# Performance work log

Hardware: AMD Instinct MI355X
Metric: run time of the kernel (lower is better)

The kernel has to match this reference:

```python
import jax, jax.numpy as jnp
import numpy as np

B, S, D, H = 2, 2048, 1024, 16  # batch, seq, d_model, num_heads
DH = D // H


def setup_inputs() -> dict:
    key = jax.random.key(0)
    ks = jax.random.split(key, 11)
    sc = 1.0 / np.sqrt(D)
    return {
        "q": jax.random.normal(ks[0], (B, S, D), jnp.float32),
        "k": jax.random.normal(ks[1], (B, S, D), jnp.float32),
        "v": jax.random.normal(ks[2], (B, S, D), jnp.float32),
        "wq": jax.random.normal(ks[3], (D, D), jnp.float32) * sc,
        "bq": jax.random.normal(ks[4], (D,), jnp.float32) * 0.01,
        "wk": jax.random.normal(ks[5], (D, D), jnp.float32) * sc,
        "bk": jax.random.normal(ks[6], (D,), jnp.float32) * 0.01,
        "wv": jax.random.normal(ks[7], (D, D), jnp.float32) * sc,
        "bv": jax.random.normal(ks[8], (D,), jnp.float32) * 0.01,
        "wo": jax.random.normal(ks[9], (D, D), jnp.float32) * sc,
        "bo": jax.random.normal(ks[10], (D,), jnp.float32) * 0.01,
    }


def reference(q, k, v, wq, bq, wk, bk, wv, bv, wo, bo):
    # projections: [B,S,D]
    query = q @ wq + bq
    key_ = k @ wk + bk
    value = v @ wv + bv
    # split heads: [B,H,S,DH]
    def split(x):
        return jnp.transpose(x.reshape(B, S, H, DH), (0, 2, 1, 3))
    query, key_, value = split(query), split(key_), split(value)
    # NOTE: original module applies NO 1/sqrt(d_k) scaling
    scores = jnp.einsum("bhqd,bhkd->bhqk", query, key_)
    attn = jax.nn.softmax(scores, axis=-1)
    data = jnp.einsum("bhqk,bhkd->bhqd", attn, value)  # [B,H,S,DH]
    # faithful to original bug: transpose(0,1) then view(B,S,-1)
    data = jnp.swapaxes(data, 0, 1).reshape(B, S, D)
    return data @ wo + bo
```

## Files before the change

kernel.cpp:

```cpp
#include <hip/hip_runtime.h>

typedef _Float16 f16;
typedef _Float16 f16x8 __attribute__((ext_vector_type(8)));
typedef _Float16 f16x4 __attribute__((ext_vector_type(4)));
typedef float    f32x4 __attribute__((ext_vector_type(4)));

static constexpr int BATCH = 2, SEQ = 2048, DMODEL = 1024, HEADS = 16, DHEAD = 64;
static constexpr int MTOK = BATCH * SEQ;
static constexpr float LOG2E = 1.44269504088896f;

#define GLOBAL_LOAD_LDS16(gptr, lptr)                                              \
  __builtin_amdgcn_global_load_lds(                                                \
      (const __attribute__((address_space(1))) void*)(gptr),                       \
      (__attribute__((address_space(3))) void*)(lptr), 16, 0, 0)

#define MFMA16(a, b, c) __builtin_amdgcn_mfma_f32_16x16x32_f16((a), (b), (c), 0, 0, 0)

#define WAITV_(N) asm volatile("s_waitcnt vmcnt(" #N ")" ::: "memory")
#define WAITV(N) WAITV_(N)

__device__ __forceinline__ float fexp2(float x) {
  float r;
  asm volatile("v_exp_f32 %0, %1" : "=v"(r) : "v"(x));
  return r;
}

__device__ __forceinline__ int imgAB(int mr, int kr) {
  int pr = mr >> 1;
  int jj = ((mr & 1) << 2) | (kr >> 3);
  int j = jj ^ (pr & 7);
  return pr * 64 + j * 8 + (kr & 7);
}
__device__ __forceinline__ int imgK(int sr, int dh) {
  return sr * 64 + (((dh >> 3) ^ (sr & 7)) << 3) + (dh & 7);
}

__global__ __launch_bounds__(256) void cast_kernel(const float* __restrict__ src,
                                                   f16* __restrict__ dst) {
  int c = blockIdx.x * 256 + threadIdx.x;
  int blk = c >> 8, cb = c & 255;
  int pr = cb >> 3, j = cb & 7;
  int jj = j ^ (pr & 7);
  int mr = (pr << 1) | (jj >> 2);
  int kr = (jj & 3) << 3;
  int m = (blk >> 5) * 64 + mr;
  int k = (blk & 31) * 32 + kr;
  const float* s = src + (size_t)m * DMODEL + k;
  f32x4 a = *(const f32x4*)s, b = *(const f32x4*)(s + 4);
  f16x8 o;
  o[0] = (f16)a[0]; o[1] = (f16)a[1]; o[2] = (f16)a[2]; o[3] = (f16)a[3];
  o[4] = (f16)b[0]; o[5] = (f16)b[1]; o[6] = (f16)b[2]; o[7] = (f16)b[3];
  *(f16x8*)(dst + (size_t)c * 8) = o;
}

__global__ __launch_bounds__(256) void transw_kernel(
    const float* __restrict__ w0, const float* __restrict__ w1,
    const float* __restrict__ w2, const float* __restrict__ w3,
    f16* __restrict__ Wimg) {
  const int z = blockIdx.z;
  const float* w = z == 0 ? w0 : z == 1 ? w1 : z == 2 ? w2 : w3;
  f16* t = Wimg + (size_t)z * DMODEL * DMODEL;
  __shared__ f16 lt[64][72];
  const int k0 = blockIdx.x * 64, n0 = blockIdx.y * 64;
  const int r = threadIdx.x >> 2, c0 = (threadIdx.x & 3) * 16;
  const float* src = w + (size_t)(k0 + r) * DMODEL + n0 + c0;
#pragma unroll
  for (int jx = 0; jx < 16; jx += 4) {
    f32x4 x = *(const f32x4*)(src + jx);
    lt[c0 + jx + 0][r] = (f16)x[0];
    lt[c0 + jx + 1][r] = (f16)x[1];
    lt[c0 + jx + 2][r] = (f16)x[2];
    lt[c0 + jx + 3][r] = (f16)x[3];
  }
  __syncthreads();
  const int n = n0 + r;
#pragma unroll
  for (int cw = 0; cw < 2; cw++) {
    int k = k0 + c0 + cw * 8;
    int blk = ((n >> 6) << 5) | (k >> 5);
    int off = blk * 2048 + imgAB(n & 63, k & 31);
    f16x8 v;
#pragma unroll
    for (int e = 0; e < 8; e++) v[e] = lt[r][c0 + cw * 8 + e];
    *(f16x8*)(t + off) = v;
  }
}

__global__ __launch_bounds__(256) void proj_kernel(
    const f16* __restrict__ Ximg, const f16* __restrict__ Wimg,
    const float* __restrict__ bq, const float* __restrict__ bk,
    const float* __restrict__ bv, f16* __restrict__ Qp, f16* __restrict__ Kp,
    f16* __restrict__ Vt, int zbase, size_t aStride) {
  __shared__ f16 As[2][4096];
  __shared__ f16 Bs[2][4096];
  const int z = zbase + blockIdx.z;
  const f16* A = Ximg + (size_t)blockIdx.z * aStride;
  const f16* Bw = Wimg + (size_t)z * DMODEL * DMODEL;
  int lin = blockIdx.x + (blockIdx.y << 3);
  int swz = ((lin & 7) << 5) + (lin >> 3);
  const int n0 = (swz & 7) * 128, m0 = (swz >> 3) * 128;
  const int tid = threadIdx.x, w = tid >> 6, l = tid & 63, q = l & 15, g = l >> 4;
  const int wr = w >> 1, wc = w & 1;
  const int KT = DMODEL >> 5;
  int aoff[4], boff[4];
#pragma unroll
  for (int mi = 0; mi < 4; mi++) {
    int mr = wr * 64 + mi * 16 + q;
    aoff[mi] = ((mr >> 6) << 11) + imgAB(mr & 63, g * 8);
  }
#pragma unroll
  for (int ni = 0; ni < 4; ni++) {
    int nr = wc * 64 + ni * 16 + q;
    boff[ni] = ((nr >> 6) << 11) + imgAB(nr & 63, g * 8);
  }
  f32x4 acc[4][4] = {};

#define PROJ_STAGE(bb, t)                                                          \
  {                                                                                \
    _Pragma("unroll")                                                              \
    for (int i = 0; i < 2; i++) {                                                  \
      int c = w * 2 + i;                                                           \
      size_t ga = (size_t)(((m0 >> 6) + (c >> 2)) * KT + (t)) * 2048 +             \
                  (c & 3) * 512 + l * 8;                                           \
      GLOBAL_LOAD_LDS16(A + ga, (char*)&As[bb][c * 512]);                          \
      size_t gb = (size_t)(((n0 >> 6) + (c >> 2)) * KT + (t)) * 2048 +             \
                  (c & 3) * 512 + l * 8;                                           \
      GLOBAL_LOAD_LDS16(Bw + gb, (char*)&Bs[bb][c * 512]);                         \
    }                                                                              \
  }

  PROJ_STAGE(0, 0);
  for (int t = 0; t < KT; t++) {
    const int bb = t & 1;
    if (t < KT - 1) {
      PROJ_STAGE(bb ^ 1, t + 1);
      WAITV(4);
    } else {
      WAITV(0);
    }
    __builtin_amdgcn_s_barrier();
    f16x8 af[4], bf[4];
#pragma unroll
    for (int mi = 0; mi < 4; mi++) af[mi] = *(const f16x8*)&As[bb][aoff[mi]];
#pragma unroll
    for (int ni = 0; ni < 4; ni++) bf[ni] = *(const f16x8*)&Bs[bb][boff[ni]];
#pragma unroll
    for (int mi = 0; mi < 4; mi++)
#pragma unroll
      for (int ni = 0; ni < 4; ni++)
        acc[mi][ni] = MFMA16(af[mi], bf[ni], acc[mi][ni]);
    __builtin_amdgcn_s_barrier();
  }
  const float* bias = z == 0 ? bq : (z == 1 ? bk : bv);
#pragma unroll
  for (int mi = 0; mi < 4; mi++)
#pragma unroll
    for (int ni = 0; ni < 4; ni++) {
      const int col = n0 + wc * 64 + ni * 16 + q;
      const float bvl = bias[col];
      const int row0 = m0 + wr * 64 + mi * 16 + g * 4;
      if (z == 0) {
#pragma unroll
        for (int r = 0; r < 4; r++)
          Qp[(size_t)(row0 + r) * DMODEL + col] = (f16)((acc[mi][ni][r] + bvl) * LOG2E);
      } else if (z == 1) {
        const int h = col >> 6, dh = col & 63;
#pragma unroll
        for (int r = 0; r < 4; r++) {
          const int row = row0 + r, s = row & (SEQ - 1);
          Kp[(size_t)(((row >> 11) * HEADS + h) * 64 + (s >> 5)) * 2048 + imgK(s & 31, dh)] =
              (f16)(acc[mi][ni][r] + bvl);
        }
      } else {
        const int h = col >> 6, dh = col & 63;
        const int s0 = row0 & (SEQ - 1);
        f16* dst = Vt + (size_t)(((row0 >> 11) * HEADS + h) * 64 + (s0 >> 5)) * 2048 +
                   imgAB(dh, s0 & 31);
        f16x4 ov;
        ov[0] = (f16)(acc[mi][ni][0] + bvl); ov[1] = (f16)(acc[mi][ni][1] + bvl);
        ov[2] = (f16)(acc[mi][ni][2] + bvl); ov[3] = (f16)(acc[mi][ni][3] + bvl);
        *(f16x4*)dst = ov;
      }
    }
}

__global__ __launch_bounds__(256, 4) void attn_kernel(
    const f16* __restrict__ Qp, const f16* __restrict__ Kimg,
    const f16* __restrict__ Vimg, f16* __restrict__ Simg) {
  __shared__ f16 Klds[2][2][2048];
  __shared__ f16 Vlds[2][2][2048];
  __shared__ f16 Plds[4][2][512];
  const int tid = threadIdx.x, w = tid >> 6, l = tid & 63, q = l & 15, g = l >> 4;
  const int lin = blockIdx.x;
  const int swz = ((lin & 7) << 7) + (lin >> 3);
  const int qb = swz & 31, bh = swz >> 5;
  const int b = bh >> 4, h = bh & 15;
  const int q0 = qb * 64 + w * 16;

  const f16* qrow = Qp + (size_t)(b * SEQ + q0 + q) * DMODEL + h * 64;
  const f16x8 qf0 = *(const f16x8*)(qrow + g * 8);
  const f16x8 qf1 = *(const f16x8*)(qrow + 32 + g * 8);
  const f16* kt_base = Kimg + (size_t)(bh * 64) * 2048;
  const f16* vt_base = Vimg + (size_t)(bh * 64) * 2048;

  int koff[4][2];
#pragma unroll
  for (int fn = 0; fn < 4; fn++)
#pragma unroll
    for (int hf = 0; hf < 2; hf++)
      koff[fn][hf] = (fn >> 1) * 2048 + imgK((fn & 1) * 16 + q, hf * 32 + g * 8);
  int voff[4];
#pragma unroll
  for (int fo = 0; fo < 4; fo++) voff[fo] = imgAB(fo * 16 + q, g * 8);
  const int poff = imgAB(q, g * 8);
  int pwoff[2];
  {
    const int pr = q >> 1;
#pragma unroll
    for (int fn = 0; fn < 2; fn++) {
      int jj = ((q & 1) << 2) | (fn * 2 + (g >> 1));
      pwoff[fn] = pr * 64 + ((jj ^ (pr & 7)) << 3) + (g & 1) * 4;
    }
  }
  float m_st = -1.0e30f, l_pt = 0.f;
  f32x4 o_acc[4] = {};

#define ATTN_STAGE(bb, t)                                                          \
  {                                                                                \
    const f16* sb_ = (w < 2) ? (kt_base + (size_t)(2 * (t) + w) * 2048)            \
                             : (vt_base + (size_t)(2 * (t) + (w - 2)) * 2048);     \
    f16* db_ = (w < 2) ? &Klds[bb][w][0] : &Vlds[bb][w - 2][0];                    \
    _Pragma("unroll")                                                              \
    for (int j_ = 0; j_ < 4; j_++)                                                 \
      GLOBAL_LOAD_LDS16(sb_ + j_ * 512 + l * 8, (char*)(db_ + j_ * 512));          \
  }

  ATTN_STAGE(0, 0);
  for (int t = 0; t < 32; t++) {
    const int bb = t & 1;
    if (t < 31) {
      ATTN_STAGE(bb ^ 1, t + 1);
      WAITV(4);
    } else {
      WAITV(0);
    }
    __builtin_amdgcn_s_barrier();
    const f16* Kb = &Klds[bb][0][0];
    f32x4 sacc[4];
#pragma unroll
    for (int fn = 0; fn < 4; fn++) {
      f32x4 zz = {};
      zz = MFMA16(*(const f16x8*)(Kb + koff[fn][0]), qf0, zz);
      zz = MFMA16(*(const f16x8*)(Kb + koff[fn][1]), qf1, zz);
      sacc[fn] = zz;
    }
    float lm = fmaxf(
        fmaxf(fmaxf(fmaxf(sacc[0][0], sacc[0][1]), fmaxf(sacc[0][2], sacc[0][3])),
              fmaxf(fmaxf(sacc[1][0], sacc[1][1]), fmaxf(sacc[1][2], sacc[1][3]))),
        fmaxf(fmaxf(fmaxf(sacc[2][0], sacc[2][1]), fmaxf(sacc[2][2], sacc[2][3])),
              fmaxf(fmaxf(sacc[3][0], sacc[3][1]), fmaxf(sacc[3][2], sacc[3][3]))));
    if (!__all(lm <= m_st + 8.f)) {
      float mx = fmaxf(lm, __shfl_xor(lm, 16, 64));
      mx = fmaxf(mx, __shfl_xor(mx, 32, 64));
      const float mnew = fmaxf(m_st, mx);
      const float sc = fexp2(m_st - mnew);
      m_st = mnew;
      l_pt *= sc;
#pragma unroll
      for (int fo = 0; fo < 4; fo++) {
        o_acc[fo][0] *= sc; o_acc[fo][1] *= sc;
        o_acc[fo][2] *= sc; o_acc[fo][3] *= sc;
      }
    }
    float ts = 0.f;
#pragma unroll
    for (int fn = 0; fn < 4; fn++) {
      f16x4 pk;
#pragma unroll
      for (int r = 0; r < 4; r++) {
        float e = fexp2(sacc[fn][r] - m_st);
        ts += e;
        pk[r] = (f16)e;
      }
      *(f16x4*)(&Plds[w][fn >> 1][0] + pwoff[fn & 1]) = pk;
    }
    l_pt += ts;
    const f16x8 p0 = *(const f16x8*)(&Plds[w][0][0] + poff);
    const f16x8 p1 = *(const f16x8*)(&Plds[w][1][0] + poff);
    const f16* Vb = &Vlds[bb][0][0];
#pragma unroll
    for (int fo = 0; fo < 4; fo++) {
      o_acc[fo] = MFMA16(*(const f16x8*)(Vb + voff[fo]), p0, o_acc[fo]);
      o_acc[fo] = MFMA16(*(const f16x8*)(Vb + 2048 + voff[fo]), p1, o_acc[fo]);
    }
    __builtin_amdgcn_s_barrier();
  }
  float lsum = l_pt + __shfl_xor(l_pt, 16, 64);
  lsum += __shfl_xor(lsum, 32, 64);
  const float inv = 1.f / lsum;
  const int s = q0 + q;
  const int m16 = (2 * h + b) & 15, bp = h >> 3;
  const int tp = bp * SEQ + m16 * 128 + (s >> 4);
#pragma unroll
  for (int fo = 0; fo < 4; fo++) {
    const int d0 = (s & 15) * 64 + fo * 16 + g * 4;
    f16* dst = Simg + (size_t)(((tp >> 6) << 5) | (d0 >> 5)) * 2048 + imgAB(tp & 63, d0 & 31);
    f16x4 ov;
    ov[0] = (f16)(o_acc[fo][0] * inv); ov[1] = (f16)(o_acc[fo][1] * inv);
    ov[2] = (f16)(o_acc[fo][2] * inv); ov[3] = (f16)(o_acc[fo][3] * inv);
    *(f16x4*)dst = ov;
  }
}

__global__ __launch_bounds__(256) void ogemm_kernel(
    const f16* __restrict__ Aimg, const f16* __restrict__ Bimg,
    const float* __restrict__ bias, float* __restrict__ out) {
  __shared__ f16 As[2][4096];
  __shared__ f16 Bs[2][2048];
  int lin = blockIdx.x + (blockIdx.y << 4);
  int swz = ((lin & 7) << 6) + (lin >> 3);
  const int n0 = (swz & 15) * 64, m0 = (swz >> 4) * 128;
  const int tid = threadIdx.x, w = tid >> 6, l = tid & 63, q = l & 15, g = l >> 4;
  const int wr = w >> 1, wc = w & 1;
  int aoff[4], boff[2];
#pragma unroll
  for (int mi = 0; mi < 4; mi++) {
    int mr = wr * 64 + mi * 16 + q;
    aoff[mi] = ((mr >> 6) << 11) + imgAB(mr & 63, g * 8);
  }
#pragma unroll
  for (int ni = 0; ni < 2; ni++) boff[ni] = imgAB(wc * 32 + ni * 16 + q, g * 8);
  f32x4 acc[4][2] = {};

#define OG_STAGE(bb, t)                                                            \
  {                                                                                \
    _Pragma("unroll")                                                              \
    for (int i = 0; i < 2; i++) {                                                  \
      int c = w * 2 + i;                                                           \
      size_t ga = (size_t)(((m0 >> 6) + (c >> 2)) * 32 + (t)) * 2048 +             \
                  (c & 3) * 512 + l * 8;                                           \
      GLOBAL_LOAD_LDS16(Aimg + ga, (char*)&As[bb][c * 512]);                       \
    }                                                                              \
    size_t gb = (size_t)((n0 >> 6) * 32 + (t)) * 2048 + w * 512 + l * 8;           \
    GLOBAL_LOAD_LDS16(Bimg + gb, (char*)&Bs[bb][w * 512]);                         \
  }

  OG_STAGE(0, 0);
  for (int t = 0; t < 32; t++) {
    const int bb = t & 1;
    if (t < 31) {
      OG_STAGE(bb ^ 1, t + 1);
      WAITV(3);
    } else {
      WAITV(0);
    }
    __builtin_amdgcn_s_barrier();
    f16x8 af[4], bf[2];
#pragma unroll
    for (int mi = 0; mi < 4; mi++) af[mi] = *(const f16x8*)&As[bb][aoff[mi]];
#pragma unroll
    for (int ni = 0; ni < 2; ni++) bf[ni] = *(const f16x8*)&Bs[bb][boff[ni]];
#pragma unroll
    for (int mi = 0; mi < 4; mi++)
#pragma unroll
      for (int ni = 0; ni < 2; ni++)
        acc[mi][ni] = MFMA16(af[mi], bf[ni], acc[mi][ni]);
    __builtin_amdgcn_s_barrier();
  }
#pragma unroll
  for (int mi = 0; mi < 4; mi++)
#pragma unroll
    for (int ni = 0; ni < 2; ni++) {
      const int col = n0 + wc * 32 + ni * 16 + q;
      const float bvl = bias[col];
      const int row0 = m0 + wr * 64 + mi * 16 + g * 4;
#pragma unroll
      for (int r = 0; r < 4; r++)
        out[(size_t)(row0 + r) * DMODEL + col] = acc[mi][ni][r] + bvl;
    }
}

extern "C" void kernel_launch(void* const* d_in, const int* in_sizes, int n_in,
                              void* d_out, int out_size, void* d_ws, size_t ws_size,
                              hipStream_t stream) {
  const float* q  = (const float*)d_in[0];
  const float* k  = (const float*)d_in[1];
  const float* v  = (const float*)d_in[2];
  const float* wq = (const float*)d_in[3];
  const float* bq = (const float*)d_in[4];
  const float* wk = (const float*)d_in[5];
  const float* bk = (const float*)d_in[6];
  const float* wv = (const float*)d_in[7];
  const float* bv = (const float*)d_in[8];
  const float* wo = (const float*)d_in[9];
  const float* bo = (const float*)d_in[10];

  const size_t XSZ = (size_t)MTOK * DMODEL;
  f16* ws = (f16*)d_ws;
  const bool fused = ws_size >= (56ull << 20);

  f16 *X0, *X1, *X2, *Qp, *Kp, *Vt, *Wimg, *scr;
  if (fused) {
    X0 = ws; X1 = ws + XSZ; X2 = ws + 2 * XSZ;
    Qp = ws + 3 * XSZ; Kp = ws + 4 * XSZ; Vt = ws + 5 * XSZ;
    Wimg = ws + 6 * XSZ;
    scr = X0;
  } else {
    X0 = X1 = X2 = ws;
    Qp = ws + XSZ; Kp = ws + 2 * XSZ; Vt = ws + 3 * XSZ;
    Wimg = ws + 4 * XSZ;
    scr = X0;
  }

  dim3 blk(256);
  dim3 gT(16, 16, 4);
  dim3 gC(2048);
  dim3 gA(1024);
  dim3 gO(16, 32);

  transw_kernel<<<gT, blk, 0, stream>>>(wq, wk, wv, wo, Wimg);

  if (fused) {
    cast_kernel<<<gC, blk, 0, stream>>>(q, X0);
    cast_kernel<<<gC, blk, 0, stream>>>(k, X1);
    cast_kernel<<<gC, blk, 0, stream>>>(v, X2);
    proj_kernel<<<dim3(8, 32, 3), blk, 0, stream>>>(X0, Wimg, bq, bk, bv, Qp, Kp, Vt, 0, XSZ);
  } else {
    cast_kernel<<<gC, blk, 0, stream>>>(q, X0);
    proj_kernel<<<dim3(8, 32, 1), blk, 0, stream>>>(X0, Wimg, bq, bk, bv, Qp, Kp, Vt, 0, 0);
    cast_kernel<<<gC, blk, 0, stream>>>(k, X0);
    proj_kernel<<<dim3(8, 32, 1), blk, 0, stream>>>(X0, Wimg, bq, bk, bv, Qp, Kp, Vt, 1, 0);
    cast_kernel<<<gC, blk, 0, stream>>>(v, X0);
    proj_kernel<<<dim3(8, 32, 1), blk, 0, stream>>>(X0, Wimg, bq, bk, bv, Qp, Kp, Vt, 2, 0);
  }

  attn_kernel<<<gA, blk, 0, stream>>>(Qp, Kp, Vt, scr);
  ogemm_kernel<<<gO, blk, 0, stream>>>(scr, Wimg + (size_t)3 * DMODEL * DMODEL, bo, (float*)d_out);
}
```

Before: 244.0 us.

## Give each attention wave two query tiles and merge the three cast launches

The attention kernel now runs two waves of 128 threads per block, and each wave handles 32 query rows as two 16-row fragments that share the same K and V fragments read from LDS. This halves LDS traffic per unit of MFMA work and lets the code hoist K/V fragment loads ahead of grouped MFMAs, with s_setprio raised around the MFMA sections. Each of the two waves now issues 8 async loads per stage instead of 4. The probability conversion uses packed cvt_pkrtz, which rounds toward zero instead of to nearest. The three cast launches become one launch with blockIdx.z selecting the tensor. Register pressure rises, and with half as many waves per block, latency hiding may suffer.

```diff
diff --git a/kernel.cpp b/kernel.cpp
--- a/kernel.cpp
+++ b/kernel.cpp
@@ -3,6 +3,7 @@
 typedef _Float16 f16;
 typedef _Float16 f16x8 __attribute__((ext_vector_type(8)));
 typedef _Float16 f16x4 __attribute__((ext_vector_type(4)));
+typedef __fp16   h16x2 __attribute__((ext_vector_type(2)));
 typedef float    f32x4 __attribute__((ext_vector_type(4)));
 
 static constexpr int BATCH = 2, SEQ = 2048, DMODEL = 1024, HEADS = 16, DHEAD = 64;
@@ -23,6 +24,9 @@
   float r;
   asm volatile("v_exp_f32 %0, %1" : "=v"(r) : "v"(x));
   return r;
+}
+__device__ __forceinline__ float m3(float a, float b, float c) {
+  return fmaxf(fmaxf(a, b), c);
 }
 
 __device__ __forceinline__ int imgAB(int mr, int kr) {
@@ -35,8 +39,13 @@
   return sr * 64 + (((dh >> 3) ^ (sr & 7)) << 3) + (dh & 7);
 }
 
-__global__ __launch_bounds__(256) void cast_kernel(const float* __restrict__ src,
-                                                   f16* __restrict__ dst) {
+__global__ __launch_bounds__(256) void cast3_kernel(
+    const float* __restrict__ qs, const float* __restrict__ ks,
+    const float* __restrict__ vs, f16* __restrict__ X0, f16* __restrict__ X1,
+    f16* __restrict__ X2) {
+  const int z = blockIdx.z;
+  const float* src = z == 0 ? qs : z == 1 ? ks : vs;
+  f16* dst = z == 0 ? X0 : z == 1 ? X1 : X2;
   int c = blockIdx.x * 256 + threadIdx.x;
   int blk = c >> 8, cb = c & 255;
   int pr = cb >> 3, j = cb & 7;
@@ -184,22 +193,26 @@
     }
 }
 
-__global__ __launch_bounds__(256, 4) void attn_kernel(
+__global__ __launch_bounds__(128, 2) void attn_kernel(
     const f16* __restrict__ Qp, const f16* __restrict__ Kimg,
     const f16* __restrict__ Vimg, f16* __restrict__ Simg) {
   __shared__ f16 Klds[2][2][2048];
   __shared__ f16 Vlds[2][2][2048];
-  __shared__ f16 Plds[4][2][512];
+  __shared__ f16 Plds[2][2][2][512];
   const int tid = threadIdx.x, w = tid >> 6, l = tid & 63, q = l & 15, g = l >> 4;
   const int lin = blockIdx.x;
   const int swz = ((lin & 7) << 7) + (lin >> 3);
   const int qb = swz & 31, bh = swz >> 5;
   const int b = bh >> 4, h = bh & 15;
-  const int q0 = qb * 64 + w * 16;
-
-  const f16* qrow = Qp + (size_t)(b * SEQ + q0 + q) * DMODEL + h * 64;
-  const f16x8 qf0 = *(const f16x8*)(qrow + g * 8);
-  const f16x8 qf1 = *(const f16x8*)(qrow + 32 + g * 8);
+  const int q0 = qb * 64 + w * 32;
+
+  const f16* qrowA = Qp + (size_t)(b * SEQ + q0 + q) * DMODEL + h * 64;
+  const f16x8 qA0 = *(const f16x8*)(qrowA + g * 8);
+  const f16x8 qA1 = *(const f16x8*)(qrowA + 32 + g * 8);
+  const f16* qrowB = qrowA + (size_t)16 * DMODEL;
+  const f16x8 qB0 = *(const f16x8*)(qrowB + g * 8);
+  const f16x8 qB1 = *(const f16x8*)(qrowB + 32 + g * 8);
+
   const f16* kt_base = Kimg + (size_t)(bh * 64) * 2048;
   const f16* vt_base = Vimg + (size_t)(bh * 64) * 2048;
 
@@ -222,17 +235,54 @@
       pwoff[fn] = pr * 64 + ((jj ^ (pr & 7)) << 3) + (g & 1) * 4;
     }
   }
-  float m_st = -1.0e30f, l_pt = 0.f;
-  f32x4 o_acc[4] = {};
+  f16* PwA = &Plds[w][0][0][0];
+  f16* PwB = &Plds[w][1][0][0];
+  float mA = -1.0e30f, mB = -1.0e30f, lA = 0.f, lB = 0.f;
+  f32x4 oA[4] = {}, oB[4] = {};
 
 #define ATTN_STAGE(bb, t)                                                          \
   {                                                                                \
-    const f16* sb_ = (w < 2) ? (kt_base + (size_t)(2 * (t) + w) * 2048)            \
-                             : (vt_base + (size_t)(2 * (t) + (w - 2)) * 2048);     \
-    f16* db_ = (w < 2) ? &Klds[bb][w][0] : &Vlds[bb][w - 2][0];                    \
+    const f16* sb_ = (w == 0) ? (kt_base + (size_t)(2 * (t)) * 2048)               \
+                              : (vt_base + (size_t)(2 * (t)) * 2048);              \
+    f16* db_ = (w == 0) ? &Klds[bb][0][0] : &Vlds[bb][0][0];                       \
     _Pragma("unroll")                                                              \
-    for (int j_ = 0; j_ < 4; j_++)                                                 \
+    for (int j_ = 0; j_ < 8; j_++)                                                 \
       GLOBAL_LOAD_LDS16(sb_ + j_ * 512 + l * 8, (char*)(db_ + j_ * 512));          \
+  }
+
+#define SOFTMAX_FRAG(s, m_st, l_pt, o, PbF)                                        \
+  {                                                                                \
+    float lm = fmaxf(m3(m3(s[0][0], s[0][1], s[0][2]),                             \
+                        m3(s[0][3], s[1][0], s[1][1]),                             \
+                        m3(s[1][2], s[1][3], s[2][0])),                            \
+                     m3(m3(s[2][1], s[2][2], s[2][3]),                             \
+                        m3(s[3][0], s[3][1], s[3][2]), s[3][3]));                  \
+    if (!__all(lm <= m_st + 8.f)) {                                                \
+      float mx = fmaxf(lm, __shfl_xor(lm, 16, 64));                                \
+      mx = fmaxf(mx, __shfl_xor(mx, 32, 64));                                      \
+      const float mnew = fmaxf(m_st, mx);                                          \
+      const float sc = fexp2(m_st - mnew);                                         \
+      m_st = mnew;                                                                 \
+      l_pt *= sc;                                                                  \
+      _Pragma("unroll")                                                            \
+      for (int fo_ = 0; fo_ < 4; fo_++) {                                          \
+        o[fo_][0] *= sc; o[fo_][1] *= sc; o[fo_][2] *= sc; o[fo_][3] *= sc;        \
+      }                                                                            \
+    }                                                                              \
+    float ts = 0.f;                                                                \
+    _Pragma("unroll")                                                              \
+    for (int fn_ = 0; fn_ < 4; fn_++) {                                            \
+      float e0 = fexp2(s[fn_][0] - m_st);                                          \
+      float e1 = fexp2(s[fn_][1] - m_st);                                          \
+      float e2 = fexp2(s[fn_][2] - m_st);                                          \
+      float e3 = fexp2(s[fn_][3] - m_st);                                          \
+      ts += (e0 + e1) + (e2 + e3);                                                 \
+      union { f16x4 v4; h16x2 h2[2]; } pu_;                                        \
+      pu_.h2[0] = __builtin_amdgcn_cvt_pkrtz(e0, e1);                              \
+      pu_.h2[1] = __builtin_amdgcn_cvt_pkrtz(e2, e3);                              \
+      *(f16x4*)((PbF) + (fn_ >> 1) * 512 + pwoff[fn_ & 1]) = pu_.v4;               \
+    }                                                                              \
+    l_pt += ts;                                                                    \
   }
 
   ATTN_STAGE(0, 0);
@@ -240,75 +290,77 @@
     const int bb = t & 1;
     if (t < 31) {
       ATTN_STAGE(bb ^ 1, t + 1);
-      WAITV(4);
+      WAITV(8);
     } else {
       WAITV(0);
     }
     __builtin_amdgcn_s_barrier();
     const f16* Kb = &Klds[bb][0][0];
-    f32x4 sacc[4];
+    f16x8 kf[4][2];
 #pragma unroll
     for (int fn = 0; fn < 4; fn++) {
-      f32x4 zz = {};
-      zz = MFMA16(*(const f16x8*)(Kb + koff[fn][0]), qf0, zz);
-      zz = MFMA16(*(const f16x8*)(Kb + koff[fn][1]), qf1, zz);
-      sacc[fn] = zz;
-    }
-    float lm = fmaxf(
-        fmaxf(fmaxf(fmaxf(sacc[0][0], sacc[0][1]), fmaxf(sacc[0][2], sacc[0][3])),
-              fmaxf(fmaxf(sacc[1][0], sacc[1][1]), fmaxf(sacc[1][2], sacc[1][3]))),
-        fmaxf(fmaxf(fmaxf(sacc[2][0], sacc[2][1]), fmaxf(sacc[2][2], sacc[2][3])),
-              fmaxf(fmaxf(sacc[3][0], sacc[3][1]), fmaxf(sacc[3][2], sacc[3][3]))));
-    if (!__all(lm <= m_st + 8.f)) {
-      float mx = fmaxf(lm, __shfl_xor(lm, 16, 64));
-      mx = fmaxf(mx, __shfl_xor(mx, 32, 64));
-      const float mnew = fmaxf(m_st, mx);
-      const float sc = fexp2(m_st - mnew);
-      m_st = mnew;
-      l_pt *= sc;
-#pragma unroll
-      for (int fo = 0; fo < 4; fo++) {
-        o_acc[fo][0] *= sc; o_acc[fo][1] *= sc;
-        o_acc[fo][2] *= sc; o_acc[fo][3] *= sc;
-      }
-    }
-    float ts = 0.f;
+      kf[fn][0] = *(const f16x8*)(Kb + koff[fn][0]);
+      kf[fn][1] = *(const f16x8*)(Kb + koff[fn][1]);
+    }
+    f32x4 sA[4], sB[4];
+    __builtin_amdgcn_s_setprio(1);
 #pragma unroll
     for (int fn = 0; fn < 4; fn++) {
-      f16x4 pk;
-#pragma unroll
-      for (int r = 0; r < 4; r++) {
-        float e = fexp2(sacc[fn][r] - m_st);
-        ts += e;
-        pk[r] = (f16)e;
-      }
-      *(f16x4*)(&Plds[w][fn >> 1][0] + pwoff[fn & 1]) = pk;
-    }
-    l_pt += ts;
-    const f16x8 p0 = *(const f16x8*)(&Plds[w][0][0] + poff);
-    const f16x8 p1 = *(const f16x8*)(&Plds[w][1][0] + poff);
+      f32x4 z0 = {};
+      z0 = MFMA16(kf[fn][0], qA0, z0);
+      z0 = MFMA16(kf[fn][1], qA1, z0);
+      sA[fn] = z0;
+      f32x4 z1 = {};
+      z1 = MFMA16(kf[fn][0], qB0, z1);
+      z1 = MFMA16(kf[fn][1], qB1, z1);
+      sB[fn] = z1;
+    }
+    __builtin_amdgcn_s_setprio(0);
+    SOFTMAX_FRAG(sA, mA, lA, oA, PwA);
+    SOFTMAX_FRAG(sB, mB, lB, oB, PwB);
+    const f16x8 pA0 = *(const f16x8*)(PwA + poff);
+    const f16x8 pA1 = *(const f16x8*)(PwA + 512 + poff);
+    const f16x8 pB0 = *(const f16x8*)(PwB + poff);
+    const f16x8 pB1 = *(const f16x8*)(PwB + 512 + poff);
     const f16* Vb = &Vlds[bb][0][0];
+    f16x8 vf[4][2];
 #pragma unroll
     for (int fo = 0; fo < 4; fo++) {
-      o_acc[fo] = MFMA16(*(const f16x8*)(Vb + voff[fo]), p0, o_acc[fo]);
-      o_acc[fo] = MFMA16(*(const f16x8*)(Vb + 2048 + voff[fo]), p1, o_acc[fo]);
-    }
-    __builtin_amdgcn_s_barrier();
-  }
-  float lsum = l_pt + __shfl_xor(l_pt, 16, 64);
-  lsum += __shfl_xor(lsum, 32, 64);
-  const float inv = 1.f / lsum;
-  const int s = q0 + q;
+      vf[fo][0] = *(const f16x8*)(Vb + voff[fo]);
+      vf[fo][1] = *(const f16x8*)(Vb + 2048 + voff[fo]);
+    }
+    __builtin_amdgcn_s_setprio(1);
+#pragma unroll
+    for (int fo = 0; fo < 4; fo++) {
+      oA[fo] = MFMA16(vf[fo][0], pA0, oA[fo]);
+      oA[fo] = MFMA16(vf[fo][1], pA1, oA[fo]);
+      oB[fo] = MFMA16(vf[fo][0], pB0, oB[fo]);
+      oB[fo] = MFMA16(vf[fo][1], pB1, oB[fo]);
+    }
+    __builtin_amdgcn_s_setprio(0);
+    __builtin_amdgcn_s_barrier();
+  }
+  float lsA = lA + __shfl_xor(lA, 16, 64);
+  lsA += __shfl_xor(lsA, 32, 64);
+  float lsB = lB + __shfl_xor(lB, 16, 64);
+  lsB += __shfl_xor(lsB, 32, 64);
+  const float invA = 1.f / lsA, invB = 1.f / lsB;
   const int m16 = (2 * h + b) & 15, bp = h >> 3;
-  const int tp = bp * SEQ + m16 * 128 + (s >> 4);
-#pragma unroll
-  for (int fo = 0; fo < 4; fo++) {
-    const int d0 = (s & 15) * 64 + fo * 16 + g * 4;
-    f16* dst = Simg + (size_t)(((tp >> 6) << 5) | (d0 >> 5)) * 2048 + imgAB(tp & 63, d0 & 31);
-    f16x4 ov;
-    ov[0] = (f16)(o_acc[fo][0] * inv); ov[1] = (f16)(o_acc[fo][1] * inv);
-    ov[2] = (f16)(o_acc[fo][2] * inv); ov[3] = (f16)(o_acc[fo][3] * inv);
-    *(f16x4*)dst = ov;
+#pragma unroll
+  for (int half = 0; half < 2; half++) {
+    const int s = q0 + half * 16 + q;
+    const int tp = bp * SEQ + m16 * 128 + (s >> 4);
+    const float inv = half ? invB : invA;
+    const f32x4* o = half ? oB : oA;
+#pragma unroll
+    for (int fo = 0; fo < 4; fo++) {
+      const int d0 = (s & 15) * 64 + fo * 16 + g * 4;
+      f16* dst = Simg + (size_t)(((tp >> 6) << 5) | (d0 >> 5)) * 2048 + imgAB(tp & 63, d0 & 31);
+      f16x4 ov;
+      ov[0] = (f16)(o[fo][0] * inv); ov[1] = (f16)(o[fo][1] * inv);
+      ov[2] = (f16)(o[fo][2] * inv); ov[3] = (f16)(o[fo][3] * inv);
+      *(f16x4*)dst = ov;
+    }
   }
 }
 
@@ -412,28 +464,25 @@
     scr = X0;
   }
 
-  dim3 blk(256);
+  dim3 blk(256), blk128(128);
   dim3 gT(16, 16, 4);
-  dim3 gC(2048);
   dim3 gA(1024);
   dim3 gO(16, 32);
 
   transw_kernel<<<gT, blk, 0, stream>>>(wq, wk, wv, wo, Wimg);
 
   if (fused) {
-    cast_kernel<<<gC, blk, 0, stream>>>(q, X0);
-    cast_kernel<<<gC, blk, 0, stream>>>(k, X1);
-    cast_kernel<<<gC, blk, 0, stream>>>(v, X2);
+    cast3_kernel<<<dim3(2048, 1, 3), blk, 0, stream>>>(q, k, v, X0, X1, X2);
     proj_kernel<<<dim3(8, 32, 3), blk, 0, stream>>>(X0, Wimg, bq, bk, bv, Qp, Kp, Vt, 0, XSZ);
   } else {
-    cast_kernel<<<gC, blk, 0, stream>>>(q, X0);
+    cast3_kernel<<<dim3(2048, 1, 1), blk, 0, stream>>>(q, q, q, X0, X0, X0);
     proj_kernel<<<dim3(8, 32, 1), blk, 0, stream>>>(X0, Wimg, bq, bk, bv, Qp, Kp, Vt, 0, 0);
-    cast_kernel<<<gC, blk, 0, stream>>>(k, X0);
+    cast3_kernel<<<dim3(2048, 1, 1), blk, 0, stream>>>(k, k, k, X0, X0, X0);
     proj_kernel<<<dim3(8, 32, 1), blk, 0, stream>>>(X0, Wimg, bq, bk, bv, Qp, Kp, Vt, 1, 0);
-    cast_kernel<<<gC, blk, 0, stream>>>(v, X0);
+    cast3_kernel<<<dim3(2048, 1, 1), blk, 0, stream>>>(v, v, v, X0, X0, X0);
     proj_kernel<<<dim3(8, 32, 1), blk, 0, stream>>>(X0, Wimg, bq, bk, bv, Qp, Kp, Vt, 2, 0);
   }
 
-  attn_kernel<<<gA, blk, 0, stream>>>(Qp, Kp, Vt, scr);
+  attn_kernel<<<gA, blk128, 0, stream>>>(Qp, Kp, Vt, scr);
   ogemm_kernel<<<gO, blk, 0, stream>>>(scr, Wimg + (size_t)3 * DMODEL * DMODEL, bo, (float*)d_out);
 }
```

Result: faster. 235.9 us (-3.3%).
